# Performance work log

Measured on AMD Instinct MI355X. Metric: run time of the kernel, lower is better.

The kernel has to match this reference:

```python
import jax, jax.numpy as jnp
import numpy as np
import math

L = 2          # n_layers
H = 12         # n_heads
D = 768        # hidden_size
S = 2048       # seq_len
BS = 128       # block_size
HALO = 32      # halo_size
INNER = 3072   # inner_size
EPS = 1e-12    # layer_norm_eps
DH = D // H    # head dim
NB = S // BS   # num blocks
WIN = BS + 2 * HALO  # key/value window per block


def _layer_norm(x, g, b):
    mu = jnp.mean(x, axis=-1, keepdims=True)
    var = jnp.mean(jnp.square(x - mu), axis=-1, keepdims=True)
    return (x - mu) * jax.lax.rsqrt(var + EPS) * g + b


def setup_inputs() -> dict:
    key = jax.random.key(0)
    ks = jax.random.split(key, 20)
    s = 0.02
    inp = {"x": jax.random.normal(ks[0], (8, S, D), jnp.float32)}
    # stacked per-layer params [L, ...]
    inp["Wq"] = jax.random.normal(ks[1], (L, D, D)) * s
    inp["bq"] = jnp.zeros((L, D))
    inp["Wk"] = jax.random.normal(ks[2], (L, D, D)) * s
    inp["bk"] = jnp.zeros((L, D))
    inp["Wv"] = jax.random.normal(ks[3], (L, D, D)) * s
    inp["bv"] = jnp.zeros((L, D))
    inp["Wo"] = jax.random.normal(ks[4], (L, D, D)) * s
    inp["bo"] = jnp.zeros((L, D))
    inp["ln1_g"] = jnp.ones((L, D))
    inp["ln1_b"] = jnp.zeros((L, D))
    inp["W1"] = jax.random.normal(ks[5], (L, D, INNER)) * s
    inp["b1"] = jnp.zeros((L, INNER))
    inp["W2"] = jax.random.normal(ks[6], (L, INNER, D)) * s
    inp["b2"] = jnp.zeros((L, D))
    inp["ln2_g"] = jnp.ones((L, D))
    inp["ln2_b"] = jnp.zeros((L, D))
    return inp


def _halo_layer(x, Wq, bq, Wk, bk, Wv, bv, Wo, bo, ln1_g, ln1_b, W1, b1, W2, b2, ln2_g, ln2_b):
    B = x.shape[0]
    # --- block-local halo attention (vectorized over blocks) ---
    # window gather via zero-padding + masking: padded positions are masked
    # to -inf in scores, which is mathematically identical to the original
    # smaller windows at the first/last block.
    xp = jnp.pad(x, ((0, 0), (HALO, HALO), (0, 0)))          # [B, S+2h, D]
    idx = (jnp.arange(NB) * BS)[:, None] + jnp.arange(WIN)[None, :]
    valid = ((idx - HALO) >= 0) & ((idx - HALO) < S)
    xw = xp[:, idx]

    q = (x @ Wq + bq).reshape(B, NB, BS, H, DH)
    k = (xw @ Wk + bk).reshape(B, NB, WIN, H, DH)
    v = (xw @ Wv + bv).reshape(B, NB, WIN, H, DH)

    scores = jnp.einsum('bnqhd,bnkhd->bnhqk', q, k) / math.sqrt(DH)
    neg = jnp.finfo(scores.dtype).min
    scores = jnp.where(valid[None, :, None, None, :], scores, neg)
    probs = jax.nn.softmax(scores, axis=-1)
    ctx = jnp.einsum('bnhqk,bnkhd->bnqhd', probs, v).reshape(B, S, D)

    attn_out = _layer_norm(ctx @ Wo + bo + x, ln1_g, ln1_b)

    # --- feed forward (gelu, exact erf form as torch default) ---
    h = jax.nn.gelu(attn_out @ W1 + b1, approximate=False)
    h = h @ W2 + b2
    return _layer_norm(h + attn_out, ln2_g, ln2_b)


def reference(x, Wq, bq, Wk, bk, Wv, bv, Wo, bo, ln1_g, ln1_b,
              W1, b1, W2, b2, ln2_g, ln2_b):
    outs = []
    h = x
    for l in range(L):
        h = _halo_layer(h, Wq[l], bq[l], Wk[l], bk[l], Wv[l], bv[l], Wo[l], bo[l],
                        ln1_g[l], ln1_b[l], W1[l], b1[l], W2[l], b2[l], ln2_g[l], ln2_b[l])
        outs.append(h)
    return jnp.stack(outs)  # [L, B, S, D] == list of all encoded layers
```

## Files before the change

kernel.cpp:

```cpp
#include <hip/hip_runtime.h>
#include <hip/hip_bf16.h>

typedef unsigned short u16;
typedef unsigned int u32;

static const int DD = 768;
static const int SS = 2048;
static const int BB = 8;
static const int HH = 12;
static const int NBLK = 16;
static const int ROWS = BB * SS;
static const size_t AD = (size_t)ROWS * DD;
static const size_t D2 = (size_t)DD * DD;
static const size_t DI = (size_t)DD * 3072;

typedef __attribute__((ext_vector_type(8))) short short8;
typedef __attribute__((ext_vector_type(4))) float f32x4;

union U16x8 { uint4 u; short8 s; };

__device__ __forceinline__ float bl(u32 u) { return __uint_as_float(u << 16); }
__device__ __forceinline__ float bh(u32 u) { return __uint_as_float(u & 0xffff0000u); }
__device__ __forceinline__ u16 f2b(float f) {
    u32 u = __float_as_uint(f);
    u += 0x7fffu + ((u >> 16) & 1u);
    return (u16)(u >> 16);
}
__device__ __forceinline__ u32 pack2(float lo, float hi) {
    return (u32)f2b(lo) | ((u32)f2b(hi) << 16);
}

__device__ __forceinline__ void gload16(const u16* g, u16* l) {
    __builtin_amdgcn_global_load_lds(
        (const __attribute__((address_space(1))) void*)g,
        (__attribute__((address_space(3))) void*)l, 16, 0, 0);
}

__device__ __forceinline__ float gelu_fast(float v) {
    float z2 = 1.5957691216f * (v + 0.044715f * v * v * v);
    z2 = fminf(z2, 80.f);
    float e = __expf(z2);
    return v * (e / (e + 1.0f));
}

__global__ __launch_bounds__(256) void cast_bf16(const float* __restrict__ x,
                                                 u16* __restrict__ xb, int n) {
    int i = (blockIdx.x * 256 + threadIdx.x) * 4;
    if (i < n) {
        float4 v = *reinterpret_cast<const float4*>(x + i);
        uint2 p;
        p.x = pack2(v.x, v.y);
        p.y = pack2(v.z, v.w);
        *reinterpret_cast<uint2*>(xb + i) = p;
    }
}

__global__ __launch_bounds__(256) void cast_transpose(const float* __restrict__ W,
                                                      u16* __restrict__ WT,
                                                      int K, int N) {
    __shared__ float tile[32][33];
    int bx = blockIdx.x;
    int by = blockIdx.y;
    int tx = threadIdx.x;
    int ty = threadIdx.y;
#pragma unroll
    for (int i = 0; i < 4; i++) {
        int kr = by * 32 + ty + i * 8;
        tile[ty + i * 8][tx] = W[(size_t)kr * N + bx * 32 + tx];
    }
    __syncthreads();
#pragma unroll
    for (int i = 0; i < 4; i++) {
        int nr = bx * 32 + ty + i * 8;
        WT[(size_t)nr * K + by * 32 + tx] = f2b(tile[tx][ty + i * 8]);
    }
}

template <int EPI>
__global__ __launch_bounds__(256, 4) void gemm128(const u16* __restrict__ A,
                                                  const u16* __restrict__ BT,
                                                  const float* __restrict__ b0,
                                                  const float* __restrict__ b1,
                                                  const float* __restrict__ b2,
                                                  void* __restrict__ C0,
                                                  void* __restrict__ C1,
                                                  void* __restrict__ C2,
                                                  int M, int N, int K, int NTN) {
    extern __shared__ u16 smem[];
    const int tid = threadIdx.x;
    const int nwg = gridDim.x;
    int wg = blockIdx.x;
    wg = (wg & 7) * (nwg >> 3) + (wg >> 3);
    const int tn = wg % NTN, tm = wg / NTN;
    const int m0 = tm * 128, n0 = tn * 128;
    const int lane = tid & 63, w = tid >> 6;
    const int wr = w >> 1, wc = w & 1;
    const int lr = lane & 15, ls = lane >> 4;
    const int sl = ls ^ ((lr >> 1) & 3);

    const int r3 = tid >> 2, c2 = tid & 3;
    const int kswz = ((c2 ^ ((r3 >> 1) & 3)) << 3);
    const u16* sA = A + (size_t)(m0 + r3) * K + kswz;
    const u16* sB = BT + (size_t)(n0 + r3) * K + kswz;
    const size_t rstep = (size_t)64 * K;

    f32x4 acc[4][4];
#pragma unroll
    for (int i = 0; i < 4; i++)
#pragma unroll
        for (int j = 0; j < 4; j++) acc[i][j] = (f32x4){0.f, 0.f, 0.f, 0.f};

#define STAGE_SLOT(SLOT)                                                      \
    {                                                                         \
        u16* pA = smem + (SLOT) * 8192 + tid * 8;                             \
        u16* pB = smem + (SLOT) * 8192 + 4096 + tid * 8;                      \
        gload16(sA, pA);                                                      \
        gload16(sA + rstep, pA + 2048);                                       \
        gload16(sB, pB);                                                      \
        gload16(sB + rstep, pB + 2048);                                       \
        sA += 32;                                                             \
        sB += 32;                                                             \
    }
#define COMPUTE_SLOT(SLOT)                                                    \
    {                                                                         \
        const u16* bufA = smem + (SLOT) * 8192 + (wr * 64 + lr) * 32;         \
        const u16* bufB = smem + (SLOT) * 8192 + 4096 + (wc * 64 + lr) * 32;  \
        U16x8 af[4], bf[4];                                                   \
        _Pragma("unroll") for (int ni = 0; ni < 4; ni++)                      \
            bf[ni].u = *(const uint4*)(bufB + ni * 512 + sl * 8);             \
        _Pragma("unroll") for (int mi = 0; mi < 4; mi++)                      \
            af[mi].u = *(const uint4*)(bufA + mi * 512 + sl * 8);             \
        _Pragma("unroll") for (int mi = 0; mi < 4; mi++)                      \
            _Pragma("unroll") for (int ni = 0; ni < 4; ni++)                  \
                acc[mi][ni] = __builtin_amdgcn_mfma_f32_16x16x32_bf16(        \
                    af[mi].s, bf[ni].s, acc[mi][ni], 0, 0, 0);                \
    }

    const int NT = K >> 5;
    STAGE_SLOT(0)
    __syncthreads();

    for (int t = 0; t < NT; t += 2) {
        if (t + 1 < NT) STAGE_SLOT(1)
        COMPUTE_SLOT(0)
        __syncthreads();
        if (t + 2 < NT) STAGE_SLOT(0)
        COMPUTE_SLOT(1)
        __syncthreads();
    }
#undef STAGE_SLOT
#undef COMPUTE_SLOT

    u16* dstQ = (u16*)C0;
    const float* bp = b0;
    int cbase = 0;
    if (EPI == 5) {
        int band = n0 / 768;
        dstQ = (band == 0) ? (u16*)C0 : (band == 1) ? (u16*)C1 : (u16*)C2;
        bp = (band == 0) ? b0 : (band == 1) ? b1 : b2;
        cbase = n0 - band * 768;
    }
#pragma unroll
    for (int mi = 0; mi < 4; mi++) {
        int row0 = m0 + wr * 64 + mi * 16 + ls * 4;
#pragma unroll
        for (int ni = 0; ni < 4; ni++) {
            int cloc = wc * 64 + ni * 16 + lr;
            float v[4];
            if (EPI == 5) {
                float bs = bp[cbase + cloc];
#pragma unroll
                for (int r = 0; r < 4; r++) {
                    v[r] = acc[mi][ni][r] + bs;
                    dstQ[(size_t)(row0 + r) * 768 + cbase + cloc] = f2b(v[r]);
                }
            } else {
                int col = n0 + cloc;
                float bs = b0[col];
#pragma unroll
                for (int r = 0; r < 4; r++) {
                    v[r] = acc[mi][ni][r] + bs;
                    if (EPI == 2) v[r] = gelu_fast(v[r]);
                    ((u16*)C0)[(size_t)(row0 + r) * N + col] = f2b(v[r]);
                }
            }
        }
    }
}

template <bool RESF32, bool OUTF32>
__global__ __launch_bounds__(256) void resid_ln2(const u16* __restrict__ a,
                                                 const void* __restrict__ res,
                                                 const float* __restrict__ g,
                                                 const float* __restrict__ be,
                                                 float* __restrict__ of,
                                                 u16* __restrict__ ob) {
    const int row = blockIdx.x * 4 + (threadIdx.x >> 6);
    const int lane = threadIdx.x & 63;
    const size_t base = (size_t)row * 768;
    float v[12];
    float s = 0.f;
#pragma unroll
    for (int i = 0; i < 3; i++) {
        int c = lane * 4 + i * 256;
        uint2 av = *reinterpret_cast<const uint2*>(a + base + c);
        float rv0, rv1, rv2, rv3;
        if (RESF32) {
            float4 r4 = *reinterpret_cast<const float4*>((const float*)res + base + c);
            rv0 = r4.x; rv1 = r4.y; rv2 = r4.z; rv3 = r4.w;
        } else {
            uint2 r2 = *reinterpret_cast<const uint2*>((const u16*)res + base + c);
            rv0 = bl(r2.x); rv1 = bh(r2.x); rv2 = bl(r2.y); rv3 = bh(r2.y);
        }
        v[i * 4 + 0] = bl(av.x) + rv0;
        v[i * 4 + 1] = bh(av.x) + rv1;
        v[i * 4 + 2] = bl(av.y) + rv2;
        v[i * 4 + 3] = bh(av.y) + rv3;
        s += v[i * 4 + 0] + v[i * 4 + 1] + v[i * 4 + 2] + v[i * 4 + 3];
    }
#pragma unroll
    for (int o = 1; o < 64; o <<= 1) s += __shfl_xor(s, o);
    float mean = s * (1.f / 768.f);
    float q = 0.f;
#pragma unroll
    for (int i = 0; i < 12; i++) {
        float d = v[i] - mean;
        q += d * d;
    }
#pragma unroll
    for (int o = 1; o < 64; o <<= 1) q += __shfl_xor(q, o);
    float inv = rsqrtf(q * (1.f / 768.f) + 1e-12f);
#pragma unroll
    for (int i = 0; i < 3; i++) {
        int c = lane * 4 + i * 256;
        float4 g4 = *reinterpret_cast<const float4*>(g + c);
        float4 b4 = *reinterpret_cast<const float4*>(be + c);
        float y0 = (v[i * 4 + 0] - mean) * inv * g4.x + b4.x;
        float y1 = (v[i * 4 + 1] - mean) * inv * g4.y + b4.y;
        float y2 = (v[i * 4 + 2] - mean) * inv * g4.z + b4.z;
        float y3 = (v[i * 4 + 3] - mean) * inv * g4.w + b4.w;
        if (OUTF32) {
            float4 o4 = {y0, y1, y2, y3};
            *reinterpret_cast<float4*>(of + base + c) = o4;
        }
        uint2 ob2;
        ob2.x = pack2(y0, y1);
        ob2.y = pack2(y2, y3);
        *reinterpret_cast<uint2*>(ob + base + c) = ob2;
    }
}

__global__ __launch_bounds__(256) void attn_mfma(const u16* __restrict__ Q,
                                                 const u16* __restrict__ Kx,
                                                 const u16* __restrict__ Vx,
                                                 u16* __restrict__ Ctx) {
    __shared__ u16 sm0[128 * 104];
    __shared__ u16 sm1[64 * 192];
    u16* Ks = sm0;
    u16* Ps = sm0;
    u16* Vs = sm1;

    const int bid = blockIdx.x;
    const int h = bid % HH;
    const int n = (bid / HH) % NBLK;
    const int b = bid / (HH * NBLK);
    const int tid = threadIdx.x;
    const int lane = tid & 63, w = tid >> 6;
    const int lr = lane & 15, ls = lane >> 4;
    const int s0 = n * 128 - 32;

#pragma unroll
    for (int j = 0; j < 6; j++) {
        int r = (tid >> 3) + j * 32;
        int c = tid & 7;
        int s = min(max(s0 + r, 0), SS - 1);
        uint4 kv = *reinterpret_cast<const uint4*>(Kx + ((size_t)(b * SS + s)) * 768 + h * 64 + c * 8);
        int byteo = r * 128 + ((c * 16) ^ ((r & 7) << 4));
        *reinterpret_cast<uint4*>(Ks + (byteo >> 1)) = kv;
    }
#pragma unroll
    for (int j = 0; j < 6; j++) {
        int r = (tid >> 3) + j * 32;
        int c = tid & 7;
        int s = min(max(s0 + r, 0), SS - 1);
        uint4 vv = *reinterpret_cast<const uint4*>(Vx + ((size_t)(b * SS + s)) * 768 + h * 64 + c * 8);
        const u16* e = reinterpret_cast<const u16*>(&vv);
        int chunk = r >> 3;
        int bo = (r & 7) * 2;
#pragma unroll
        for (int i = 0; i < 8; i++) {
            int d = c * 8 + i;
            int pch = chunk ^ (d & 7) ^ ((d >> 3) & 7);
            Vs[(d * 384 + pch * 16 + bo) >> 1] = e[i];
        }
    }
    __syncthreads();

    const int qrow0 = b * SS + n * 128 + w * 32;
    U16x8 qf[2][2];
#pragma unroll
    for (int mi = 0; mi < 2; mi++)
#pragma unroll
        for (int ks = 0; ks < 2; ks++)
            qf[mi][ks].u = *reinterpret_cast<const uint4*>(
                Q + (size_t)(qrow0 + mi * 16 + lr) * 768 + h * 64 + ks * 32 + ls * 8);

    f32x4 sc[2][12];
#pragma unroll
    for (int mi = 0; mi < 2; mi++)
#pragma unroll
        for (int jt = 0; jt < 12; jt++) sc[mi][jt] = (f32x4){0.f, 0.f, 0.f, 0.f};
#pragma unroll
    for (int jt = 0; jt < 12; jt++) {
        U16x8 kf[2];
#pragma unroll
        for (int ks = 0; ks < 2; ks++) {
            int r = jt * 16 + lr;
            int byteo = r * 128 + ((ks * 64 + ls * 16) ^ ((r & 7) << 4));
            kf[ks].u = *reinterpret_cast<const uint4*>(Ks + (byteo >> 1));
        }
#pragma unroll
        for (int mi = 0; mi < 2; mi++)
#pragma unroll
            for (int ks = 0; ks < 2; ks++)
                sc[mi][jt] = __builtin_amdgcn_mfma_f32_16x16x32_bf16(
                    qf[mi][ks].s, kf[ks].s, sc[mi][jt], 0, 0, 0);
    }

    const int lo = (n == 0) ? 32 : 0;
    const int hi = (n == NBLK - 1) ? 160 : 192;
    float mx[2][4], sm[2][4], inv[2][4];
#pragma unroll
    for (int mi = 0; mi < 2; mi++)
#pragma unroll
        for (int r = 0; r < 4; r++) { mx[mi][r] = -3.0e38f; sm[mi][r] = 0.f; }
#pragma unroll
    for (int jt = 0; jt < 12; jt++) {
        int col = jt * 16 + lr;
        bool valid = (col >= lo) && (col < hi);
#pragma unroll
        for (int mi = 0; mi < 2; mi++)
#pragma unroll
            for (int r = 0; r < 4; r++) {
                float v = valid ? sc[mi][jt][r] * 0.125f : -3.0e38f;
                sc[mi][jt][r] = v;
                mx[mi][r] = fmaxf(mx[mi][r], v);
            }
    }
#pragma unroll
    for (int o = 1; o <= 8; o <<= 1)
#pragma unroll
        for (int mi = 0; mi < 2; mi++)
#pragma unroll
            for (int r = 0; r < 4; r++)
                mx[mi][r] = fmaxf(mx[mi][r], __shfl_xor(mx[mi][r], o));
#pragma unroll
    for (int jt = 0; jt < 12; jt++)
#pragma unroll
        for (int mi = 0; mi < 2; mi++)
#pragma unroll
            for (int r = 0; r < 4; r++) {
                float p = __expf(sc[mi][jt][r] - mx[mi][r]);
                sc[mi][jt][r] = p;
                sm[mi][r] += p;
            }
#pragma unroll
    for (int o = 1; o <= 8; o <<= 1)
#pragma unroll
        for (int mi = 0; mi < 2; mi++)
#pragma unroll
            for (int r = 0; r < 4; r++)
                sm[mi][r] += __shfl_xor(sm[mi][r], o);
#pragma unroll
    for (int mi = 0; mi < 2; mi++)
#pragma unroll
        for (int r = 0; r < 4; r++) inv[mi][r] = 1.0f / sm[mi][r];

    f32x4 oacc[2][4];
#pragma unroll
    for (int mi = 0; mi < 2; mi++)
#pragma unroll
        for (int dt = 0; dt < 4; dt++) oacc[mi][dt] = (f32x4){0.f, 0.f, 0.f, 0.f};
    __syncthreads();

#pragma unroll
    for (int ph = 0; ph < 2; ph++) {
#pragma unroll
        for (int jj = 0; jj < 6; jj++) {
            int jt = ph * 6 + jj;
#pragma unroll
            for (int mi = 0; mi < 2; mi++) {
                int row = w * 32 + mi * 16 + ls * 4;
#pragma unroll
                for (int r = 0; r < 4; r++)
                    Ps[(row + r) * 104 + jj * 16 + lr] = f2b(sc[mi][jt][r]);
            }
        }
        __syncthreads();
#pragma unroll
        for (int kk = 0; kk < 3; kk++) {
            U16x8 pf[2], vf[4];
#pragma unroll
            for (int mi = 0; mi < 2; mi++)
                pf[mi].u = *reinterpret_cast<const uint4*>(
                    Ps + (w * 32 + mi * 16 + lr) * 104 + kk * 32 + ls * 8);
#pragma unroll
            for (int dt = 0; dt < 4; dt++) {
                int rrow = dt * 16 + lr;
                int lch = ph * 12 + kk * 4 + ls;
                int pch = lch ^ (rrow & 7) ^ ((rrow >> 3) & 7);
                vf[dt].u = *reinterpret_cast<const uint4*>(Vs + ((rrow * 384 + pch * 16) >> 1));
            }
#pragma unroll
            for (int mi = 0; mi < 2; mi++)
#pragma unroll
                for (int dt = 0; dt < 4; dt++)
                    oacc[mi][dt] = __builtin_amdgcn_mfma_f32_16x16x32_bf16(
                        pf[mi].s, vf[dt].s, oacc[mi][dt], 0, 0, 0);
        }
        __syncthreads();
    }

#pragma unroll
    for (int mi = 0; mi < 2; mi++)
#pragma unroll
        for (int dt = 0; dt < 4; dt++)
#pragma unroll
            for (int r = 0; r < 4; r++) {
                float v = oacc[mi][dt][r] * inv[mi][r];
                Ctx[(size_t)(qrow0 + mi * 16 + ls * 4 + r) * 768 + h * 64 + dt * 16 + lr] = f2b(v);
            }
}

extern "C" void kernel_launch(void* const* d_in, const int* in_sizes, int n_in,
                              void* d_out, int out_size, void* d_ws, size_t ws_size,
                              hipStream_t stream) {
    (void)in_sizes; (void)n_in; (void)out_size; (void)ws_size;
    const float* x    = (const float*)d_in[0];
    const float* Wq   = (const float*)d_in[1];
    const float* bq   = (const float*)d_in[2];
    const float* Wk   = (const float*)d_in[3];
    const float* bk   = (const float*)d_in[4];
    const float* Wv   = (const float*)d_in[5];
    const float* bv   = (const float*)d_in[6];
    const float* Wo   = (const float*)d_in[7];
    const float* bo   = (const float*)d_in[8];
    const float* ln1g = (const float*)d_in[9];
    const float* ln1b = (const float*)d_in[10];
    const float* W1   = (const float*)d_in[11];
    const float* b1   = (const float*)d_in[12];
    const float* W2   = (const float*)d_in[13];
    const float* b2   = (const float*)d_in[14];
    const float* ln2g = (const float*)d_in[15];
    const float* ln2b = (const float*)d_in[16];
    float* out = (float*)d_out;

    char* ws = (char*)d_ws;
    size_t off = 0;
    auto alloc = [&](size_t bytes) -> char* {
        char* p = ws + off;
        off += (bytes + 255) & ~(size_t)255;
        return p;
    };
    u16* WqkvT = (u16*)alloc(2 * 3 * D2 * sizeof(u16));
    u16* WoT   = (u16*)alloc(2 * D2 * sizeof(u16));
    u16* W1T   = (u16*)alloc(2 * DI * sizeof(u16));
    u16* W2T   = (u16*)alloc(2 * DI * sizeof(u16));
    u16* Xb    = (u16*)alloc(AD * sizeof(u16));
    u16* RegA  = (u16*)alloc(4 * AD * sizeof(u16));
    u16*   AttnB = (u16*)alloc(AD * sizeof(u16));
    u16*   H2b   = (u16*)alloc(AD * sizeof(u16));
    u16* Qb = RegA;
    u16* Kb = RegA + AD;
    u16* Vb = RegA + 2 * AD;
    u16* Ctxb = RegA + 3 * AD;
    u16* H1b = RegA;

    {
        int nelem = ROWS * DD;
        cast_bf16<<<dim3(nelem / 4 / 256), dim3(256), 0, stream>>>(x, Xb, nelem);
    }
    for (int l = 0; l < 2; l++) {
        u16* base = WqkvT + (size_t)l * 3 * D2;
        cast_transpose<<<dim3(24, 24), dim3(32, 8), 0, stream>>>(Wq + l * D2, base, 768, 768);
        cast_transpose<<<dim3(24, 24), dim3(32, 8), 0, stream>>>(Wk + l * D2, base + D2, 768, 768);
        cast_transpose<<<dim3(24, 24), dim3(32, 8), 0, stream>>>(Wv + l * D2, base + 2 * D2, 768, 768);
        cast_transpose<<<dim3(24, 24), dim3(32, 8), 0, stream>>>(Wo + l * D2, WoT + l * D2, 768, 768);
        cast_transpose<<<dim3(96, 24), dim3(32, 8), 0, stream>>>(W1 + l * DI, W1T + l * DI, 768, 3072);
        cast_transpose<<<dim3(24, 96), dim3(32, 8), 0, stream>>>(W2 + l * DI, W2T + l * DI, 3072, 768);
    }

    const size_t LDSB = 32768;
    const float* xres = x;
    for (int l = 0; l < 2; l++) {
        gemm128<5><<<dim3(128 * 18), 256, LDSB, stream>>>(
            Xb, WqkvT + (size_t)l * 3 * D2, bq + l * 768, bk + l * 768, bv + l * 768,
            Qb, Kb, Vb, ROWS, 2304, 768, 18);
        attn_mfma<<<dim3(BB * NBLK * HH), 256, 0, stream>>>(Qb, Kb, Vb, Ctxb);
        gemm128<0><<<dim3(128 * 6), 256, LDSB, stream>>>(
            Ctxb, WoT + l * D2, bo + l * 768, nullptr, nullptr,
            H2b, nullptr, nullptr, ROWS, 768, 768, 6);
        resid_ln2<true, false><<<dim3(ROWS / 4), 256, 0, stream>>>(
            H2b, (const void*)xres, ln1g + l * 768, ln1b + l * 768, nullptr, AttnB);
        gemm128<2><<<dim3(128 * 24), 256, LDSB, stream>>>(
            AttnB, W1T + l * DI, b1 + l * 3072, nullptr, nullptr,
            H1b, nullptr, nullptr, ROWS, 3072, 768, 24);
        gemm128<0><<<dim3(128 * 6), 256, LDSB, stream>>>(
            H1b, W2T + l * DI, b2 + l * 768, nullptr, nullptr,
            H2b, nullptr, nullptr, ROWS, 768, 3072, 6);
        float* outl = out + (size_t)l * AD;
        resid_ln2<false, true><<<dim3(ROWS / 4), 256, 0, stream>>>(
            H2b, (const void*)AttnB, ln2g + l * 768, ln2b + l * 768, outl, Xb);
        xres = outl;
    }
}
```

Baseline: 822.1 us.

## Load GEMM B-operand fragments directly from global into registers, bypassing LDS

The GEMM kernel no longer stages the weight (B) tile through shared memory. Each wave now loads its B fragments straight from global memory into double-buffered registers one k-step ahead, which halves LDS usage and drops the launch-bounds occupancy hint from 4 to 3. The aim is to cut LDS traffic and shared-memory footprint. The cost is that B data shared between the two row-waves is fetched twice from global/L2, the per-lane loads are uncoalesced strided row reads, and register pressure goes up.

```diff
diff --git a/kernel.cpp b/kernel.cpp
--- a/kernel.cpp
+++ b/kernel.cpp
@@ -77,7 +77,7 @@
 }
 
 template <int EPI>
-__global__ __launch_bounds__(256, 4) void gemm128(const u16* __restrict__ A,
+__global__ __launch_bounds__(256, 3) void gemm128(const u16* __restrict__ A,
                                                   const u16* __restrict__ BT,
                                                   const float* __restrict__ b0,
                                                   const float* __restrict__ b1,
@@ -101,54 +101,65 @@
     const int r3 = tid >> 2, c2 = tid & 3;
     const int kswz = ((c2 ^ ((r3 >> 1) & 3)) << 3);
     const u16* sA = A + (size_t)(m0 + r3) * K + kswz;
-    const u16* sB = BT + (size_t)(n0 + r3) * K + kswz;
     const size_t rstep = (size_t)64 * K;
 
+    const u16* bRow = BT + (size_t)(n0 + wc * 64 + lr) * K + ls * 8;
+    const size_t bStride = (size_t)16 * K;
+
     f32x4 acc[4][4];
 #pragma unroll
     for (int i = 0; i < 4; i++)
 #pragma unroll
         for (int j = 0; j < 4; j++) acc[i][j] = (f32x4){0.f, 0.f, 0.f, 0.f};
+
+    U16x8 bfA[4], bfB[4];
 
 #define STAGE_SLOT(SLOT)                                                      \
     {                                                                         \
-        u16* pA = smem + (SLOT) * 8192 + tid * 8;                             \
-        u16* pB = smem + (SLOT) * 8192 + 4096 + tid * 8;                      \
+        u16* pA = smem + (SLOT) * 4096 + tid * 8;                             \
         gload16(sA, pA);                                                      \
         gload16(sA + rstep, pA + 2048);                                       \
-        gload16(sB, pB);                                                      \
-        gload16(sB + rstep, pB + 2048);                                       \
         sA += 32;                                                             \
-        sB += 32;                                                             \
-    }
-#define COMPUTE_SLOT(SLOT)                                                    \
+    }
+#define LOAD_B(DST, KT)                                                       \
     {                                                                         \
-        const u16* bufA = smem + (SLOT) * 8192 + (wr * 64 + lr) * 32;         \
-        const u16* bufB = smem + (SLOT) * 8192 + 4096 + (wc * 64 + lr) * 32;  \
-        U16x8 af[4], bf[4];                                                   \
-        _Pragma("unroll") for (int ni = 0; ni < 4; ni++)                      \
-            bf[ni].u = *(const uint4*)(bufB + ni * 512 + sl * 8);             \
+        const u16* _bp = bRow + (size_t)(KT) * 32;                            \
+        DST[0].u = *(const uint4*)(_bp);                                      \
+        DST[1].u = *(const uint4*)(_bp + bStride);                            \
+        DST[2].u = *(const uint4*)(_bp + 2 * bStride);                        \
+        DST[3].u = *(const uint4*)(_bp + 3 * bStride);                        \
+    }
+#define COMPUTE_SLOT(SLOT, BF)                                                \
+    {                                                                         \
+        const u16* bufA = smem + (SLOT) * 4096 + (wr * 64 + lr) * 32;         \
+        U16x8 af[4];                                                          \
         _Pragma("unroll") for (int mi = 0; mi < 4; mi++)                      \
             af[mi].u = *(const uint4*)(bufA + mi * 512 + sl * 8);             \
         _Pragma("unroll") for (int mi = 0; mi < 4; mi++)                      \
             _Pragma("unroll") for (int ni = 0; ni < 4; ni++)                  \
                 acc[mi][ni] = __builtin_amdgcn_mfma_f32_16x16x32_bf16(        \
-                    af[mi].s, bf[ni].s, acc[mi][ni], 0, 0, 0);                \
+                    af[mi].s, BF[ni].s, acc[mi][ni], 0, 0, 0);                \
     }
 
     const int NT = K >> 5;
     STAGE_SLOT(0)
+    LOAD_B(bfA, 0)
     __syncthreads();
 
     for (int t = 0; t < NT; t += 2) {
+        const int k1 = (t + 1 < NT) ? t + 1 : NT - 1;
+        const int k2 = (t + 2 < NT) ? t + 2 : NT - 1;
         if (t + 1 < NT) STAGE_SLOT(1)
-        COMPUTE_SLOT(0)
+        LOAD_B(bfB, k1)
+        COMPUTE_SLOT(0, bfA)
         __syncthreads();
         if (t + 2 < NT) STAGE_SLOT(0)
-        COMPUTE_SLOT(1)
+        LOAD_B(bfA, k2)
+        COMPUTE_SLOT(1, bfB)
         __syncthreads();
     }
 #undef STAGE_SLOT
+#undef LOAD_B
 #undef COMPUTE_SLOT
 
     u16* dstQ = (u16*)C0;
@@ -490,7 +501,7 @@
         cast_transpose<<<dim3(24, 96), dim3(32, 8), 0, stream>>>(W2 + l * DI, W2T + l * DI, 3072, 768);
     }
 
-    const size_t LDSB = 32768;
+    const size_t LDSB = 16384;
     const float* xres = x;
     for (int l = 0; l < 2; l++) {
         gemm128<5><<<dim3(128 * 18), 256, LDSB, stream>>>(
```

Measured after the change: 1.202 ms. 46.2% more time.
